# Optimization experiments

Hardware: AMD Instinct MI355X
Metric: run time of the kernel (lower is better)

The kernel has to match this reference:

```python
import jax, jax.numpy as jnp
import numpy as np
from jax import lax

ENC_DIM, DEC_DIM, ATT_DIM, CONV_CH, KSIZE, ATT_ODIM = 1024, 1024, 512, 32, 50, 1024
SCALING = 2.0


def setup_inputs() -> dict:
    key = jax.random.key(0)
    ks = jax.random.split(key, 12)
    B, T = 32, 2000
    enc_pad = jax.random.normal(ks[0], (B, T, ENC_DIM), dtype=jnp.float32)
    enc_len = jax.random.randint(ks[1], (B,), 1000, T + 1, dtype=jnp.int32)
    dec_h = jax.random.normal(ks[2], (B, 1, DEC_DIM), dtype=jnp.float32)
    att_prev = jax.random.uniform(ks[3], (B, T), dtype=jnp.float32)
    s = 0.02
    W_enc = jax.random.normal(ks[4], (ENC_DIM, ATT_DIM), dtype=jnp.float32) * s
    b_enc = jnp.zeros((ATT_DIM,), jnp.float32)
    W_dec = jax.random.normal(ks[5], (DEC_DIM, ATT_DIM), dtype=jnp.float32) * s
    b_dec = jnp.zeros((ATT_DIM,), jnp.float32)
    W_att = jax.random.normal(ks[6], (CONV_CH, ATT_DIM), dtype=jnp.float32) * s
    b_att = jnp.zeros((ATT_DIM,), jnp.float32)
    # Conv2d(1, C, kernel=(1, 2K+1)) acting on (B,1,1,T) == 1D conv kernel (C,1,2K+1)
    conv_w = jax.random.normal(ks[7], (CONV_CH, 1, 2 * KSIZE + 1), dtype=jnp.float32) * s
    gvec = jax.random.normal(ks[8], (ATT_DIM, 1), dtype=jnp.float32) * s
    W_o = jax.random.normal(ks[9], (ENC_DIM, ATT_ODIM), dtype=jnp.float32) * s
    b_o = jnp.zeros((ATT_ODIM,), jnp.float32)
    return {"enc_pad": enc_pad, "enc_len": enc_len, "dec_h": dec_h, "att_prev": att_prev,
            "W_enc": W_enc, "b_enc": b_enc, "W_dec": W_dec, "b_dec": b_dec,
            "W_att": W_att, "b_att": b_att, "conv_w": conv_w, "gvec": gvec,
            "W_o": W_o, "b_o": b_o}


def reference(enc_pad, enc_len, dec_h, att_prev, W_enc, b_enc, W_dec, b_dec,
              W_att, b_att, conv_w, gvec, W_o, b_o):
    B, T, _ = enc_pad.shape
    enc_h = enc_pad @ W_enc + b_enc                           # [B,T,A]
    # location conv: (B,1,T) * (C,1,K) -> (B,C,T), SAME padding
    att_conv = lax.conv_general_dilated(
        att_prev[:, None, :], conv_w, window_strides=(1,),
        padding=[(KSIZE, KSIZE)], dimension_numbers=("NCH", "OIH", "NCH"))
    att_conv = jnp.transpose(att_conv, (0, 2, 1)) @ W_att + b_att  # [B,T,A]
    dec_term = (dec_h.reshape(B, DEC_DIM) @ W_dec + b_dec)[:, None, :]  # [B,1,A]
    att_state = jnp.tanh(enc_h + dec_term + att_conv)         # [B,T,A]
    e = (att_state @ gvec)[:, :, 0]                           # [B,T]
    mask = jnp.arange(T)[None, :] >= enc_len[:, None]         # True = padded
    e = jnp.where(mask, jnp.float32(-1e15), e)
    attn = jax.nn.softmax(SCALING * e, axis=1)                # [B,T]
    c = jnp.einsum("bt,btd->bd", attn, enc_pad)               # [B,enc_dim]
    c = c @ W_o + b_o                                         # [B,att_odim]
    return c, attn
```

## Files before the change

### kernel.cpp

```cpp
#include <hip/hip_runtime.h>
#include <stdint.h>
#include <stddef.h>

#define T_LEN   2000
#define BATCH   32
#define ROWS    64000
#define KDIM    1024
#define ADIM    512
#define CCH     32
#define KW      101

typedef _Float16 half8_t  __attribute__((ext_vector_type(8)));
typedef _Float16 half4_t  __attribute__((ext_vector_type(4)));
typedef float    float4_t __attribute__((ext_vector_type(4)));

__device__ __forceinline__ half8_t pack8(float4_t a, float4_t b) {
    half8_t r;
    r[0] = (_Float16)a.x; r[1] = (_Float16)a.y;
    r[2] = (_Float16)a.z; r[3] = (_Float16)a.w;
    r[4] = (_Float16)b.x; r[5] = (_Float16)b.y;
    r[6] = (_Float16)b.z; r[7] = (_Float16)b.w;
    return r;
}

__device__ __forceinline__ float tanh_fast(float x) {
    float ax = __builtin_fabsf(x);
    ax = fminf(ax, 15.f);
    float e = __expf(2.f * ax);
    float t = 1.f - 2.f * __builtin_amdgcn_rcpf(e + 1.f);
    return (x < 0.f) ? -t : t;
}

__device__ __forceinline__ void glds16(const void* g, void* l) {
    __builtin_amdgcn_global_load_lds((const __attribute__((address_space(1))) uint32_t*)g,
                                     (__attribute__((address_space(3))) uint32_t*)l,
                                     16, 0, 0);
}

#define OFF_WENCT 0
#define OFF_WATTT 1048576
#define OFF_CONV  1081344
#define M_DTERM   5177344
#define M_EPART   5242880
#define M_CPART   6266880
#define M_ENCH    8364032
#define F_DTERM   9273344
#define F_EPART   9338880
#define F_CPART   10362880

__global__ __launch_bounds__(256) void k_prep(const float* __restrict__ We,
                                              const float* __restrict__ Wa,
                                              const float* __restrict__ dec_h,
                                              const float* __restrict__ W_dec,
                                              const float* __restrict__ be,
                                              const float* __restrict__ bd,
                                              const float* __restrict__ ba,
                                              const float* __restrict__ att_prev,
                                              const float* __restrict__ conv_w,
                                              const float* __restrict__ enc,
                                              _Float16* __restrict__ Wet,
                                              _Float16* __restrict__ Wat,
                                              float* __restrict__ dterm,
                                              void* __restrict__ convO,
                                              _Float16* __restrict__ encH,
                                              int f16mode) {
    __shared__ float smem[3460];
    const int blk = blockIdx.x, tid = threadIdx.x;

    if (blk >= 1153) {
        const size_t idx = (size_t)(blk - 1153) * 2048 + tid * 8;
        const float4_t* s = (const float4_t*)(enc + idx);
        float4_t v0 = s[0], v1 = s[1];
        *(half8_t*)(encH + idx) = pack8(v0, v1);
        return;
    }
    if (blk < 512) {
        float (*tile)[33] = (float(*)[33])smem;
        const int k0 = (blk >> 4) * 32, n0 = (blk & 15) * 32;
        const int tx = tid & 31, ty = tid >> 5;
#pragma unroll
        for (int i = 0; i < 4; ++i)
            tile[ty + i * 8][tx] = We[(size_t)(k0 + ty + i * 8) * ADIM + n0 + tx];
        __syncthreads();
#pragma unroll
        for (int i = 0; i < 4; ++i)
            Wet[(size_t)(n0 + ty + i * 8) * KDIM + k0 + tx] = (_Float16)tile[tx][ty + i * 8];
    } else if (blk < 640) {
        float* dh = smem;
        float* part = smem + 1024;
        const int idx = blk - 512, b = idx >> 2, a0 = (idx & 3) * 128;
#pragma unroll
        for (int i = 0; i < 4; ++i) dh[tid + i * 256] = dec_h[b * KDIM + tid + i * 256];
        __syncthreads();
        const int a = a0 + (tid & 127), kh = (tid >> 7) * 512;
        float s = 0.f;
#pragma unroll 8
        for (int k = 0; k < 512; ++k) s += dh[kh + k] * W_dec[(size_t)(kh + k) * ADIM + a];
        part[tid] = s;
        __syncthreads();
        if (tid < 128) {
            const int aa = a0 + tid;
            dterm[b * ADIM + aa] = part[tid] + part[tid + 128] + be[aa] + bd[aa] + ba[aa];
        }
    } else if (blk < 1152) {
        float* ap = smem;
        float* w  = smem + 228;
        const int idx = blk - 640, b = idx >> 4, tt = idx & 15;
        const int t0 = tt * 128;
        for (int i = tid; i < 228; i += 256) {
            int t = t0 - 50 + i;
            ap[i] = (t >= 0 && t < T_LEN) ? att_prev[b * T_LEN + t] : 0.f;
        }
        for (int i = tid; i < CCH * KW; i += 256) w[i] = conv_w[i];
        __syncthreads();
        for (int idx2 = tid; idx2 < 128 * CCH; idx2 += 256) {
            int tl = idx2 >> 5, c = idx2 & 31;
            int t = t0 + tl;
            if (t < T_LEN) {
                float s = 0.f;
#pragma unroll
                for (int j = 0; j < KW; ++j) s += ap[tl + j] * w[c * KW + j];
                const size_t o = (size_t)(b * T_LEN + t) * CCH + c;
                if (f16mode) ((_Float16*)convO)[o] = (_Float16)s;
                else         ((float*)convO)[o] = s;
            }
        }
    } else {
#pragma unroll
        for (int rr = 0; rr < 2; ++rr) {
            const int n = tid * 2 + rr;
#pragma unroll
            for (int c = 0; c < CCH; ++c)
                Wat[n * CCH + c] = (_Float16)Wa[c * ADIM + n];
        }
    }
}

template<bool F16A>
__global__ __launch_bounds__(256, F16A ? 4 : 3)
void k_gemm_e(const void* __restrict__ encv,
              const _Float16* __restrict__ Wet,
              const void* __restrict__ convv,
              const _Float16* __restrict__ Wat,
              const float* __restrict__ dterm,
              const float* __restrict__ gvec,
              float* __restrict__ epart) {
    constexpr int ABYTES = F16A ? 8192 : 16384;
    __shared__ __attribute__((aligned(16))) char     Ab[2][ABYTES];
    __shared__ __attribute__((aligned(16))) _Float16 Bh[2][128 * 32];

    const int tid  = threadIdx.x;
    const int blk  = blockIdx.x;
    int nc, mt;
    if (blk < 1984) { nc = (blk >> 3) & 3; mt = (blk >> 5) * 8 + (blk & 7); }
    else            { int r = blk - 1984; nc = r >> 2; mt = 496 + (r & 3); }
    const int m0 = mt * 128, n0 = nc * 128;

    const int wave = tid >> 6, lane = tid & 63;
    const int quad = lane >> 4, c16 = lane & 15;
    const int wm = (wave >> 1) * 64, wn = (wave & 1) * 64;

    const int rlB = lane & 15, sgB = lane >> 4;
    const int rlA = F16A ? (lane & 15) : (lane & 7);
    const int sgA = F16A ? (lane >> 4) : (lane >> 3);
    constexpr int AISS = F16A ? 2 : 4;
    constexpr int ARPC = F16A ? 16 : 8;
    constexpr int AEPS = F16A ? 8 : 4;

    const _Float16* encH = (const _Float16*)encv;
    const float*    encF = (const float*)encv;
    const _Float16* cvH  = (const _Float16*)convv;
    const float*    cvF  = (const float*)convv;

    const size_t aRow = (size_t)(m0 + wave * 32 + rlA);
    const size_t bRow = (size_t)(n0 + wave * 32 + rlB);

    float g[4], dt0[4], dt1[4];
    const int b0 = m0 / T_LEN, b1 = (m0 + 127) / T_LEN;
    const int lim = (b0 + 1) * T_LEN;
#pragma unroll
    for (int j = 0; j < 4; ++j) {
        const int col = n0 + wn + j * 16 + c16;
        g[j]   = gvec[col];
        dt0[j] = dterm[b0 * ADIM + col];
        dt1[j] = dterm[b1 * ADIM + col];
    }

    float4_t acc[4][4];
#pragma unroll
    for (int i = 0; i < 4; ++i)
#pragma unroll
        for (int j = 0; j < 4; ++j) acc[i][j] = (float4_t){0.f, 0.f, 0.f, 0.f};

#define STAGE_A(buf, base, stride, k0)                                              \
    _Pragma("unroll")                                                               \
    for (int i = 0; i < AISS; ++i)                                                  \
        glds16((base) + ((aRow + i * ARPC) * (stride)) + (k0) + sgA * AEPS,         \
               &Ab[buf][(wave * AISS + i) * 1024]);
#define STAGE_B(buf, base, stride, k0)                                              \
    _Pragma("unroll")                                                               \
    for (int i = 0; i < 2; ++i)                                                     \
        glds16((base) + ((bRow + i * 16) * (stride)) + (k0) + sgB * 8,              \
               (char*)&Bh[buf][0] + (wave * 2 + i) * 1024);

    if (F16A) { STAGE_A(0, encH, KDIM, 0) } else { STAGE_A(0, encF, KDIM, 0) }
    STAGE_B(0, Wet, KDIM, 0)
    __syncthreads();

    for (int kk = 0; kk < 33; ++kk) {
        const int cur = kk & 1, nxt = cur ^ 1;
        if (kk < 31) {
            const int kn = (kk + 1) * 32;
            if (F16A) { STAGE_A(nxt, encH, KDIM, kn) } else { STAGE_A(nxt, encF, KDIM, kn) }
            STAGE_B(nxt, Wet, KDIM, kn)
        } else if (kk == 31) {
            if (F16A) { STAGE_A(nxt, cvH, CCH, 0) } else { STAGE_A(nxt, cvF, CCH, 0) }
            STAGE_B(nxt, Wat, CCH, 0)
        }
        half8_t af[4], bf[4];
        if (F16A) {
            const _Float16* Ah = (const _Float16*)Ab[cur];
#pragma unroll
            for (int i = 0; i < 4; ++i) {
                const int row = wm + i * 16 + c16;
                af[i] = *(const half8_t*)(Ah + (row >> 4) * 512 + (quad * 16 + c16) * 8);
            }
        } else {
            const float* Afp = (const float*)Ab[cur];
#pragma unroll
            for (int i = 0; i < 4; ++i) {
                const int row = wm + i * 16 + c16;
                const float* cb = Afp + (row >> 3) * 256 + (row & 7) * 4;
                float4_t u0 = *(const float4_t*)(cb + (2 * quad) * 32);
                float4_t u1 = *(const float4_t*)(cb + (2 * quad + 1) * 32);
                af[i] = pack8(u0, u1);
            }
        }
#pragma unroll
        for (int j = 0; j < 4; ++j) {
            const int row = wn + j * 16 + c16;
            bf[j] = *(const half8_t*)(&Bh[cur][0] + (row >> 4) * 512 + (quad * 16 + c16) * 8);
        }
#pragma unroll
        for (int i = 0; i < 4; ++i)
#pragma unroll
            for (int j = 0; j < 4; ++j)
                acc[i][j] = __builtin_amdgcn_mfma_f32_16x16x32_f16(af[i], bf[j], acc[i][j], 0, 0, 0);
        __syncthreads();
    }

    float* e_lds = (float*)&Bh[0][0];
#pragma unroll
    for (int i = 0; i < 4; ++i) {
#pragma unroll
        for (int r = 0; r < 4; ++r) {
            const int rloc = wm + i * 16 + quad * 4 + r;
            const bool hi = (m0 + rloc) >= lim;
            float s = 0.f;
#pragma unroll
            for (int j = 0; j < 4; ++j)
                s += tanh_fast(acc[i][j][r] + (hi ? dt1[j] : dt0[j])) * g[j];
#pragma unroll
            for (int off = 1; off < 16; off <<= 1) s += __shfl_xor(s, off);
            if (c16 == 0) e_lds[rloc * 2 + (wave & 1)] = s;
        }
    }
    __syncthreads();
    if (tid < 128) {
        const float2 q = ((const float2*)e_lds)[tid];
        epart[nc * ROWS + m0 + tid] = q.x + q.y;
    }
#undef STAGE_A
#undef STAGE_B
}

__global__ __launch_bounds__(512) void k_softmax(const float* __restrict__ epart,
                                                 const int* __restrict__ enc_len,
                                                 float* __restrict__ attn) {
    __shared__ float ex[T_LEN];
    __shared__ float red[8];
    const int b = blockIdx.x, tid = threadIdx.x;
    const int len = enc_len[b];
    float lmax = -3.4e38f;
    for (int t = tid; t < T_LEN; t += 512) {
        float e = epart[b * T_LEN + t] + epart[ROWS + b * T_LEN + t]
                + epart[2 * ROWS + b * T_LEN + t] + epart[3 * ROWS + b * T_LEN + t];
        float lg = (t < len) ? 2.f * e : -2e15f;
        ex[t] = lg;
        lmax = fmaxf(lmax, lg);
    }
    for (int off = 1; off < 64; off <<= 1) lmax = fmaxf(lmax, __shfl_xor(lmax, off));
    if ((tid & 63) == 0) red[tid >> 6] = lmax;
    __syncthreads();
    const float m = fmaxf(fmaxf(fmaxf(red[0], red[1]), fmaxf(red[2], red[3])),
                          fmaxf(fmaxf(red[4], red[5]), fmaxf(red[6], red[7])));
    float lsum = 0.f;
    for (int t = tid; t < T_LEN; t += 512) {
        float p = __expf(ex[t] - m);
        ex[t] = p;
        lsum += p;
    }
    for (int off = 1; off < 64; off <<= 1) lsum += __shfl_xor(lsum, off);
    __syncthreads();
    if ((tid & 63) == 0) red[tid >> 6] = lsum;
    __syncthreads();
    const float inv = 1.f / (red[0] + red[1] + red[2] + red[3] + red[4] + red[5] + red[6] + red[7]);
    for (int t = tid; t < T_LEN; t += 512) attn[b * T_LEN + t] = ex[t] * inv;
}

__global__ __launch_bounds__(256) void k_cpart_h(const float* __restrict__ attn,
                                                 const _Float16* __restrict__ encH,
                                                 float* __restrict__ cpart) {
    const int b = blockIdx.y, tc = blockIdx.x, tid = threadIdx.x;
    const int t0 = tc * 125;
    float4_t s = (float4_t){0.f, 0.f, 0.f, 0.f};
    const half4_t* ep = (const half4_t*)(encH + (size_t)b * T_LEN * KDIM) + tid;
    const float* ap = attn + b * T_LEN + t0;
#pragma unroll 5
    for (int tt = 0; tt < 125; ++tt) {
        const float w = ap[tt];
        half4_t v = ep[(size_t)(t0 + tt) * 256];
        s.x += w * (float)v[0]; s.y += w * (float)v[1];
        s.z += w * (float)v[2]; s.w += w * (float)v[3];
    }
    *(float4_t*)&cpart[(size_t)(tc * BATCH + b) * KDIM + tid * 4] = s;
}

__global__ __launch_bounds__(256) void k_cpart_f(const float* __restrict__ attn,
                                                 const float* __restrict__ enc,
                                                 float* __restrict__ cpart) {
    const int b = blockIdx.y, tc = blockIdx.x, tid = threadIdx.x;
    const int t0 = tc * 125;
    float4_t s = (float4_t){0.f, 0.f, 0.f, 0.f};
    const float4_t* ep = (const float4_t*)(enc + (size_t)b * T_LEN * KDIM) + tid;
    const float* ap = attn + b * T_LEN + t0;
#pragma unroll 5
    for (int tt = 0; tt < 125; ++tt) {
        const float w = ap[tt];
        float4_t v = ep[(size_t)(t0 + tt) * 256];
        s += v * w;
    }
    *(float4_t*)&cpart[(size_t)(tc * BATCH + b) * KDIM + tid * 4] = s;
}

__global__ __launch_bounds__(256) void k_out(const float* __restrict__ cpart,
                                             const float* __restrict__ W_o,
                                             const float* __restrict__ b_o,
                                             float* __restrict__ out_c) {
    __shared__ float cm[KDIM];
    const int b = blockIdx.x, tid = threadIdx.x;
    for (int d = tid; d < KDIM; d += 256) {
        float s = 0.f;
#pragma unroll
        for (int p = 0; p < 16; ++p) s += cpart[(size_t)(p * BATCH + b) * KDIM + d];
        cm[d] = s;
    }
    __syncthreads();
    const int o = blockIdx.y * 256 + tid;
    float s = b_o[o];
#pragma unroll 8
    for (int d = 0; d < KDIM; ++d) s += cm[d] * W_o[(size_t)d * KDIM + o];
    out_c[b * KDIM + o] = s;
}

extern "C" void kernel_launch(void* const* d_in, const int* in_sizes, int n_in,
                              void* d_out, int out_size, void* d_ws, size_t ws_size,
                              hipStream_t stream) {
    const float* enc      = (const float*)d_in[0];
    const int*   enc_len  = (const int*)d_in[1];
    const float* dec_h    = (const float*)d_in[2];
    const float* att_prev = (const float*)d_in[3];
    const float* W_enc    = (const float*)d_in[4];
    const float* b_enc    = (const float*)d_in[5];
    const float* W_dec    = (const float*)d_in[6];
    const float* b_dec    = (const float*)d_in[7];
    const float* W_att    = (const float*)d_in[8];
    const float* b_att    = (const float*)d_in[9];
    const float* conv_w   = (const float*)d_in[10];
    const float* gvec     = (const float*)d_in[11];
    const float* W_o      = (const float*)d_in[12];
    const float* b_o      = (const float*)d_in[13];

    float* out_c    = (float*)d_out;
    float* out_attn = out_c + BATCH * KDIM;

    char* ws = (char*)d_ws;
    _Float16* Wet = (_Float16*)(ws + OFF_WENCT);
    _Float16* Wat = (_Float16*)(ws + OFF_WATTT);

    const size_t needMain = (size_t)M_ENCH + (size_t)ROWS * KDIM * 2;
    const bool f16p = ws_size >= needMain;

    if (f16p) {
        _Float16* convH = (_Float16*)(ws + OFF_CONV);
        float*    dterm = (float*)(ws + M_DTERM);
        float*    epart = (float*)(ws + M_EPART);
        float*    cpart = (float*)(ws + M_CPART);
        _Float16* encH  = (_Float16*)(ws + M_ENCH);

        k_prep<<<1153 + 32000, 256, 0, stream>>>(W_enc, W_att, dec_h, W_dec, b_enc, b_dec,
                                                 b_att, att_prev, conv_w, enc,
                                                 Wet, Wat, dterm, convH, encH, 1);
        k_gemm_e<true><<<2000, 256, 0, stream>>>(encH, Wet, convH, Wat, dterm, gvec, epart);
        k_softmax<<<BATCH, 512, 0, stream>>>(epart, enc_len, out_attn);
        k_cpart_h<<<dim3(16, BATCH), 256, 0, stream>>>(out_attn, encH, cpart);
        k_out<<<dim3(BATCH, 4), 256, 0, stream>>>(cpart, W_o, b_o, out_c);
    } else {
        float* convF = (float*)(ws + OFF_CONV);
        float* dterm = (float*)(ws + F_DTERM);
        float* epart = (float*)(ws + F_EPART);
        float* cpart = (float*)(ws + F_CPART);

        k_prep<<<1153, 256, 0, stream>>>(W_enc, W_att, dec_h, W_dec, b_enc, b_dec,
                                         b_att, att_prev, conv_w, enc,
                                         Wet, Wat, dterm, convF, (_Float16*)nullptr, 0);
        k_gemm_e<false><<<2000, 256, 0, stream>>>(enc, Wet, convF, Wat, dterm, gvec, epart);
        k_softmax<<<BATCH, 512, 0, stream>>>(epart, enc_len, out_attn);
        k_cpart_f<<<dim3(16, BATCH), 256, 0, stream>>>(out_attn, enc, cpart);
        k_out<<<dim3(BATCH, 4), 256, 0, stream>>>(cpart, W_o, b_o, out_c);
    }
}
```

Measured before the change: 611.9 us.

## Triple-buffer fp16 GEMM pipeline with vmcnt waits and coarsen fp16 conversion blocks

The fp16 GEMM path becomes a dedicated kernel with three LDS stages, two stages prefetched ahead. It waits with explicit s_waitcnt vmcnt plus a raw barrier instead of a full __syncthreads per K step, so global loads overlap more MFMA work. The fp32 fallback is split into its own kernel. The enc fp32-to-fp16 conversion blocks each handle four chunks, cutting that launch from 32000 to 8000 blocks. The larger LDS footprint (48KB) may lower occupancy, and the hand-placed vmcnt counts must match the number of glds16 issues per stage.

```diff
diff --git a/kernel.cpp b/kernel.cpp
--- a/kernel.cpp
+++ b/kernel.cpp
@@ -68,10 +68,13 @@
     const int blk = blockIdx.x, tid = threadIdx.x;
 
     if (blk >= 1153) {
-        const size_t idx = (size_t)(blk - 1153) * 2048 + tid * 8;
-        const float4_t* s = (const float4_t*)(enc + idx);
-        float4_t v0 = s[0], v1 = s[1];
-        *(half8_t*)(encH + idx) = pack8(v0, v1);
+        const size_t base = (size_t)(blk - 1153) * 8192 + (size_t)tid * 8;
+#pragma unroll
+        for (int i = 0; i < 4; ++i) {
+            const size_t idx = base + (size_t)i * 2048;
+            const float4_t* s = (const float4_t*)(enc + idx);
+            *(half8_t*)(encH + idx) = pack8(s[0], s[1]);
+        }
         return;
     }
     if (blk < 512) {
@@ -136,18 +139,16 @@
     }
 }
 
-template<bool F16A>
-__global__ __launch_bounds__(256, F16A ? 4 : 3)
-void k_gemm_e(const void* __restrict__ encv,
-              const _Float16* __restrict__ Wet,
-              const void* __restrict__ convv,
-              const _Float16* __restrict__ Wat,
-              const float* __restrict__ dterm,
-              const float* __restrict__ gvec,
-              float* __restrict__ epart) {
-    constexpr int ABYTES = F16A ? 8192 : 16384;
-    __shared__ __attribute__((aligned(16))) char     Ab[2][ABYTES];
-    __shared__ __attribute__((aligned(16))) _Float16 Bh[2][128 * 32];
+__global__ __launch_bounds__(256, 3)
+void k_gemm3(const _Float16* __restrict__ encH,
+             const _Float16* __restrict__ Wet,
+             const _Float16* __restrict__ cvH,
+             const _Float16* __restrict__ Wat,
+             const float* __restrict__ dterm,
+             const float* __restrict__ gvec,
+             float* __restrict__ epart) {
+    __shared__ __attribute__((aligned(16))) char     Ab[3][8192];
+    __shared__ __attribute__((aligned(16))) _Float16 Bh[3][4096];
 
     const int tid  = threadIdx.x;
     const int blk  = blockIdx.x;
@@ -159,21 +160,10 @@
     const int wave = tid >> 6, lane = tid & 63;
     const int quad = lane >> 4, c16 = lane & 15;
     const int wm = (wave >> 1) * 64, wn = (wave & 1) * 64;
-
-    const int rlB = lane & 15, sgB = lane >> 4;
-    const int rlA = F16A ? (lane & 15) : (lane & 7);
-    const int sgA = F16A ? (lane >> 4) : (lane >> 3);
-    constexpr int AISS = F16A ? 2 : 4;
-    constexpr int ARPC = F16A ? 16 : 8;
-    constexpr int AEPS = F16A ? 8 : 4;
-
-    const _Float16* encH = (const _Float16*)encv;
-    const float*    encF = (const float*)encv;
-    const _Float16* cvH  = (const _Float16*)convv;
-    const float*    cvF  = (const float*)convv;
-
-    const size_t aRow = (size_t)(m0 + wave * 32 + rlA);
-    const size_t bRow = (size_t)(n0 + wave * 32 + rlB);
+    const int rl = lane & 15, sg = lane >> 4;
+
+    const size_t aRow = (size_t)(m0 + wave * 32 + rl);
+    const size_t bRow = (size_t)(n0 + wave * 32 + rl);
 
     float g[4], dt0[4], dt1[4];
     const int b0 = m0 / T_LEN, b1 = (m0 + 127) / T_LEN;
@@ -192,18 +182,141 @@
 #pragma unroll
         for (int j = 0; j < 4; ++j) acc[i][j] = (float4_t){0.f, 0.f, 0.f, 0.f};
 
+#define STG(bf, s)                                                                  \
+    {                                                                               \
+        if ((s) < 32) {                                                             \
+            const int kn = (s) * 32;                                                \
+            _Pragma("unroll")                                                       \
+            for (int i = 0; i < 2; ++i)                                             \
+                glds16(encH + (aRow + (size_t)(i * 16)) * KDIM + kn + sg * 8,       \
+                       &Ab[bf][(wave * 2 + i) * 1024]);                             \
+            _Pragma("unroll")                                                       \
+            for (int i = 0; i < 2; ++i)                                             \
+                glds16(Wet + (bRow + (size_t)(i * 16)) * KDIM + kn + sg * 8,        \
+                       (char*)&Bh[bf][0] + (wave * 2 + i) * 1024);                  \
+        } else {                                                                    \
+            _Pragma("unroll")                                                       \
+            for (int i = 0; i < 2; ++i)                                             \
+                glds16(cvH + (aRow + (size_t)(i * 16)) * CCH + sg * 8,              \
+                       &Ab[bf][(wave * 2 + i) * 1024]);                             \
+            _Pragma("unroll")                                                       \
+            for (int i = 0; i < 2; ++i)                                             \
+                glds16(Wat + (bRow + (size_t)(i * 16)) * CCH + sg * 8,              \
+                       (char*)&Bh[bf][0] + (wave * 2 + i) * 1024);                  \
+        }                                                                           \
+    }
+
+    STG(0, 0)
+    STG(1, 1)
+
+    for (int kk = 0; kk < 33; ++kk) {
+        if (kk < 32) asm volatile("s_waitcnt vmcnt(4)" ::: "memory");
+        else         asm volatile("s_waitcnt vmcnt(0)" ::: "memory");
+        __builtin_amdgcn_s_barrier();
+        __builtin_amdgcn_sched_barrier(0);
+
+        const int s = kk + 2;
+        if (s <= 32) { const int bf = s - (s / 3) * 3; STG(bf, s) }
+
+        const int cur = kk - (kk / 3) * 3;
+        const _Float16* Ah = (const _Float16*)Ab[cur];
+        const _Float16* Bp = &Bh[cur][0];
+        half8_t af[4], bf4[4];
+#pragma unroll
+        for (int i = 0; i < 4; ++i)
+            af[i] = *(const half8_t*)(Ah + ((wm + i * 16) >> 4) * 512 + lane * 8);
+#pragma unroll
+        for (int j = 0; j < 4; ++j)
+            bf4[j] = *(const half8_t*)(Bp + ((wn + j * 16) >> 4) * 512 + lane * 8);
+#pragma unroll
+        for (int i = 0; i < 4; ++i)
+#pragma unroll
+            for (int j = 0; j < 4; ++j)
+                acc[i][j] = __builtin_amdgcn_mfma_f32_16x16x32_f16(af[i], bf4[j], acc[i][j], 0, 0, 0);
+    }
+#undef STG
+    __syncthreads();
+
+    float* e_lds = (float*)&Bh[0][0];
+#pragma unroll
+    for (int i = 0; i < 4; ++i) {
+#pragma unroll
+        for (int r = 0; r < 4; ++r) {
+            const int rloc = wm + i * 16 + quad * 4 + r;
+            const bool hi = (m0 + rloc) >= lim;
+            float s = 0.f;
+#pragma unroll
+            for (int j = 0; j < 4; ++j)
+                s += tanh_fast(acc[i][j][r] + (hi ? dt1[j] : dt0[j])) * g[j];
+#pragma unroll
+            for (int off = 1; off < 16; off <<= 1) s += __shfl_xor(s, off);
+            if (c16 == 0) e_lds[rloc * 2 + (wave & 1)] = s;
+        }
+    }
+    __syncthreads();
+    if (tid < 128) {
+        const float2 q = ((const float2*)e_lds)[tid];
+        epart[nc * ROWS + m0 + tid] = q.x + q.y;
+    }
+}
+
+__global__ __launch_bounds__(256, 3)
+void k_gemm_f(const float* __restrict__ encF,
+              const _Float16* __restrict__ Wet,
+              const float* __restrict__ cvF,
+              const _Float16* __restrict__ Wat,
+              const float* __restrict__ dterm,
+              const float* __restrict__ gvec,
+              float* __restrict__ epart) {
+    __shared__ __attribute__((aligned(16))) char     Ab[2][16384];
+    __shared__ __attribute__((aligned(16))) _Float16 Bh[2][128 * 32];
+
+    const int tid  = threadIdx.x;
+    const int blk  = blockIdx.x;
+    int nc, mt;
+    if (blk < 1984) { nc = (blk >> 3) & 3; mt = (blk >> 5) * 8 + (blk & 7); }
+    else            { int r = blk - 1984; nc = r >> 2; mt = 496 + (r & 3); }
+    const int m0 = mt * 128, n0 = nc * 128;
+
+    const int wave = tid >> 6, lane = tid & 63;
+    const int quad = lane >> 4, c16 = lane & 15;
+    const int wm = (wave >> 1) * 64, wn = (wave & 1) * 64;
+
+    const int rlB = lane & 15, sgB = lane >> 4;
+    const int rlA = lane & 7,  sgA = lane >> 3;
+
+    const size_t aRow = (size_t)(m0 + wave * 32 + rlA);
+    const size_t bRow = (size_t)(n0 + wave * 32 + rlB);
+
+    float g[4], dt0[4], dt1[4];
+    const int b0 = m0 / T_LEN, b1 = (m0 + 127) / T_LEN;
+    const int lim = (b0 + 1) * T_LEN;
+#pragma unroll
+    for (int j = 0; j < 4; ++j) {
+        const int col = n0 + wn + j * 16 + c16;
+        g[j]   = gvec[col];
+        dt0[j] = dterm[b0 * ADIM + col];
+        dt1[j] = dterm[b1 * ADIM + col];
+    }
+
+    float4_t acc[4][4];
+#pragma unroll
+    for (int i = 0; i < 4; ++i)
+#pragma unroll
+        for (int j = 0; j < 4; ++j) acc[i][j] = (float4_t){0.f, 0.f, 0.f, 0.f};
+
 #define STAGE_A(buf, base, stride, k0)                                              \
     _Pragma("unroll")                                                               \
-    for (int i = 0; i < AISS; ++i)                                                  \
-        glds16((base) + ((aRow + i * ARPC) * (stride)) + (k0) + sgA * AEPS,         \
-               &Ab[buf][(wave * AISS + i) * 1024]);
+    for (int i = 0; i < 4; ++i)                                                     \
+        glds16((base) + ((aRow + i * 8) * (stride)) + (k0) + sgA * 4,               \
+               &Ab[buf][(wave * 4 + i) * 1024]);
 #define STAGE_B(buf, base, stride, k0)                                              \
     _Pragma("unroll")                                                               \
     for (int i = 0; i < 2; ++i)                                                     \
         glds16((base) + ((bRow + i * 16) * (stride)) + (k0) + sgB * 8,              \
                (char*)&Bh[buf][0] + (wave * 2 + i) * 1024);
 
-    if (F16A) { STAGE_A(0, encH, KDIM, 0) } else { STAGE_A(0, encF, KDIM, 0) }
+    STAGE_A(0, encF, KDIM, 0)
     STAGE_B(0, Wet, KDIM, 0)
     __syncthreads();
 
@@ -211,30 +324,21 @@
         const int cur = kk & 1, nxt = cur ^ 1;
         if (kk < 31) {
             const int kn = (kk + 1) * 32;
-            if (F16A) { STAGE_A(nxt, encH, KDIM, kn) } else { STAGE_A(nxt, encF, KDIM, kn) }
+            STAGE_A(nxt, encF, KDIM, kn)
             STAGE_B(nxt, Wet, KDIM, kn)
         } else if (kk == 31) {
-            if (F16A) { STAGE_A(nxt, cvH, CCH, 0) } else { STAGE_A(nxt, cvF, CCH, 0) }
+            STAGE_A(nxt, cvF, CCH, 0)
             STAGE_B(nxt, Wat, CCH, 0)
         }
         half8_t af[4], bf[4];
-        if (F16A) {
-            const _Float16* Ah = (const _Float16*)Ab[cur];
-#pragma unroll
-            for (int i = 0; i < 4; ++i) {
-                const int row = wm + i * 16 + c16;
-                af[i] = *(const half8_t*)(Ah + (row >> 4) * 512 + (quad * 16 + c16) * 8);
-            }
-        } else {
-            const float* Afp = (const float*)Ab[cur];
-#pragma unroll
-            for (int i = 0; i < 4; ++i) {
-                const int row = wm + i * 16 + c16;
-                const float* cb = Afp + (row >> 3) * 256 + (row & 7) * 4;
-                float4_t u0 = *(const float4_t*)(cb + (2 * quad) * 32);
-                float4_t u1 = *(const float4_t*)(cb + (2 * quad + 1) * 32);
-                af[i] = pack8(u0, u1);
-            }
+        const float* Afp = (const float*)Ab[cur];
+#pragma unroll
+        for (int i = 0; i < 4; ++i) {
+            const int row = wm + i * 16 + c16;
+            const float* cb = Afp + (row >> 3) * 256 + (row & 7) * 4;
+            float4_t u0 = *(const float4_t*)(cb + (2 * quad) * 32);
+            float4_t u1 = *(const float4_t*)(cb + (2 * quad + 1) * 32);
+            af[i] = pack8(u0, u1);
         }
 #pragma unroll
         for (int j = 0; j < 4; ++j) {
@@ -248,6 +352,8 @@
                 acc[i][j] = __builtin_amdgcn_mfma_f32_16x16x32_f16(af[i], bf[j], acc[i][j], 0, 0, 0);
         __syncthreads();
     }
+#undef STAGE_A
+#undef STAGE_B
 
     float* e_lds = (float*)&Bh[0][0];
 #pragma unroll
@@ -270,8 +376,6 @@
         const float2 q = ((const float2*)e_lds)[tid];
         epart[nc * ROWS + m0 + tid] = q.x + q.y;
     }
-#undef STAGE_A
-#undef STAGE_B
 }
 
 __global__ __launch_bounds__(512) void k_softmax(const float* __restrict__ epart,
@@ -398,10 +502,10 @@
         float*    cpart = (float*)(ws + M_CPART);
         _Float16* encH  = (_Float16*)(ws + M_ENCH);
 
-        k_prep<<<1153 + 32000, 256, 0, stream>>>(W_enc, W_att, dec_h, W_dec, b_enc, b_dec,
-                                                 b_att, att_prev, conv_w, enc,
-                                                 Wet, Wat, dterm, convH, encH, 1);
-        k_gemm_e<true><<<2000, 256, 0, stream>>>(encH, Wet, convH, Wat, dterm, gvec, epart);
+        k_prep<<<1153 + 8000, 256, 0, stream>>>(W_enc, W_att, dec_h, W_dec, b_enc, b_dec,
+                                                b_att, att_prev, conv_w, enc,
+                                                Wet, Wat, dterm, convH, encH, 1);
+        k_gemm3<<<2000, 256, 0, stream>>>(encH, Wet, convH, Wat, dterm, gvec, epart);
         k_softmax<<<BATCH, 512, 0, stream>>>(epart, enc_len, out_attn);
         k_cpart_h<<<dim3(16, BATCH), 256, 0, stream>>>(out_attn, encH, cpart);
         k_out<<<dim3(BATCH, 4), 256, 0, stream>>>(cpart, W_o, b_o, out_c);
@@ -414,7 +518,7 @@
         k_prep<<<1153, 256, 0, stream>>>(W_enc, W_att, dec_h, W_dec, b_enc, b_dec,
                                          b_att, att_prev, conv_w, enc,
                                          Wet, Wat, dterm, convF, (_Float16*)nullptr, 0);
-        k_gemm_e<false><<<2000, 256, 0, stream>>>(enc, Wet, convF, Wat, dterm, gvec, epart);
+        k_gemm_f<<<2000, 256, 0, stream>>>(enc, Wet, convF, Wat, dterm, gvec, epart);
         k_softmax<<<BATCH, 512, 0, stream>>>(epart, enc_len, out_attn);
         k_cpart_f<<<dim3(16, BATCH), 256, 0, stream>>>(out_attn, enc, cpart);
         k_out<<<dim3(BATCH, 4), 256, 0, stream>>>(cpart, W_o, b_o, out_c);
```

Measured after the change: 637.0 us. +4.1%, slower.

## Add triple-buffered direct-to-LDS fp16 GEMM kernel for attention energies

Applied to the files above, without the earlier changes.

Replaces the fp16 energy GEMM with a new kernel that stages A tiles into a three-slot LDS ring and B tiles into a double buffer, using direct global-to-LDS loads. Only one barrier is taken per k-step, and the conv/W_att contribution is folded in as a 33rd k-step. The aim is deeper prefetch, so that global latency is hidden behind the MFMA work. The extra LDS buffer raises shared memory use per block, and the vmcnt accounting must stay correct for the pipeline to remain valid.

```diff
diff --git a/kernel.cpp b/kernel.cpp
--- a/kernel.cpp
+++ b/kernel.cpp
@@ -136,6 +136,135 @@
     }
 }
 
+__global__ __launch_bounds__(256, 4)
+void k_gemm_p(const _Float16* __restrict__ encH,
+              const _Float16* __restrict__ Wet,
+              const _Float16* __restrict__ cvH,
+              const _Float16* __restrict__ Wat,
+              const float* __restrict__ dterm,
+              const float* __restrict__ gvec,
+              float* __restrict__ epart) {
+    __shared__ __attribute__((aligned(16))) char Ab[3][8192];
+    __shared__ __attribute__((aligned(16))) char Bh[2][8192];
+
+    const int tid  = threadIdx.x;
+    const int blk  = blockIdx.x;
+    int nc, mt;
+    if (blk < 1984) { nc = (blk >> 3) & 3; mt = (blk >> 5) * 8 + (blk & 7); }
+    else            { int r = blk - 1984; nc = r >> 2; mt = 496 + (r & 3); }
+    const int m0 = mt * 128, n0 = nc * 128;
+
+    const int wave = tid >> 6, lane = tid & 63;
+    const int quad = lane >> 4, c16 = lane & 15;
+    const int wm = (wave >> 1) * 64, wn = (wave & 1) * 64;
+    const int rl = lane & 15, sg = lane >> 4;
+
+    const size_t aRow = (size_t)(m0 + wave * 32 + rl);
+    const size_t bRow = (size_t)(n0 + wave * 32 + rl);
+
+    float g[4], dt0[4], dt1[4];
+    const int b0 = m0 / T_LEN, b1 = (m0 + 127) / T_LEN;
+    const int lim = (b0 + 1) * T_LEN;
+#pragma unroll
+    for (int j = 0; j < 4; ++j) {
+        const int col = n0 + wn + j * 16 + c16;
+        g[j]   = gvec[col];
+        dt0[j] = dterm[b0 * ADIM + col];
+        dt1[j] = dterm[b1 * ADIM + col];
+    }
+
+    float4_t acc[4][4];
+#pragma unroll
+    for (int i = 0; i < 4; ++i)
+#pragma unroll
+        for (int j = 0; j < 4; ++j) acc[i][j] = (float4_t){0.f, 0.f, 0.f, 0.f};
+
+#define STG_A(s)                                                                     \
+    {                                                                                \
+        const int bf = (s) - ((s) / 3) * 3;                                          \
+        if ((s) < 32) {                                                              \
+            const int kn = (s) * 32;                                                 \
+            glds16(encH + (aRow +  0) * KDIM + kn + sg * 8, &Ab[bf][(wave*2+0)*1024]); \
+            glds16(encH + (aRow + 16) * KDIM + kn + sg * 8, &Ab[bf][(wave*2+1)*1024]); \
+        } else {                                                                     \
+            glds16(cvH + (aRow +  0) * CCH + sg * 8, &Ab[bf][(wave*2+0)*1024]);      \
+            glds16(cvH + (aRow + 16) * CCH + sg * 8, &Ab[bf][(wave*2+1)*1024]);      \
+        }                                                                            \
+    }
+#define STG_B(s)                                                                     \
+    {                                                                                \
+        const int bf = (s) & 1;                                                      \
+        if ((s) < 32) {                                                              \
+            const int kn = (s) * 32;                                                 \
+            glds16(Wet + (bRow +  0) * KDIM + kn + sg * 8, &Bh[bf][(wave*2+0)*1024]); \
+            glds16(Wet + (bRow + 16) * KDIM + kn + sg * 8, &Bh[bf][(wave*2+1)*1024]); \
+        } else {                                                                     \
+            glds16(Wat + (bRow +  0) * CCH + sg * 8, &Bh[bf][(wave*2+0)*1024]);      \
+            glds16(Wat + (bRow + 16) * CCH + sg * 8, &Bh[bf][(wave*2+1)*1024]);      \
+        }                                                                            \
+    }
+
+    STG_B(0)
+    STG_A(0)
+    STG_A(1)
+
+    for (int kk = 0; kk < 33; ++kk) {
+        if (kk < 32) asm volatile("s_waitcnt vmcnt(2)" ::: "memory");
+        else         asm volatile("s_waitcnt vmcnt(0)" ::: "memory");
+        __builtin_amdgcn_s_barrier();
+        __builtin_amdgcn_sched_barrier(0);
+
+        if (kk + 1 <= 32) STG_B(kk + 1)
+        if (kk + 2 <= 32) STG_A(kk + 2)
+
+        const int cur3 = kk - (kk / 3) * 3;
+        const int cur2 = kk & 1;
+        const _Float16* Ah = (const _Float16*)Ab[cur3];
+        const _Float16* Bp = (const _Float16*)Bh[cur2];
+        half8_t af[4], bf4[4];
+#pragma unroll
+        for (int i = 0; i < 4; ++i) {
+            const int row = wm + i * 16 + c16;
+            af[i] = *(const half8_t*)(Ah + (row >> 4) * 512 + (quad * 16 + c16) * 8);
+        }
+#pragma unroll
+        for (int j = 0; j < 4; ++j) {
+            const int row = wn + j * 16 + c16;
+            bf4[j] = *(const half8_t*)(Bp + (row >> 4) * 512 + (quad * 16 + c16) * 8);
+        }
+#pragma unroll
+        for (int i = 0; i < 4; ++i)
+#pragma unroll
+            for (int j = 0; j < 4; ++j)
+                acc[i][j] = __builtin_amdgcn_mfma_f32_16x16x32_f16(af[i], bf4[j], acc[i][j], 0, 0, 0);
+    }
+#undef STG_A
+#undef STG_B
+    __syncthreads();
+
+    float* e_lds = (float*)&Bh[0][0];
+#pragma unroll
+    for (int i = 0; i < 4; ++i) {
+#pragma unroll
+        for (int r = 0; r < 4; ++r) {
+            const int rloc = wm + i * 16 + quad * 4 + r;
+            const bool hi = (m0 + rloc) >= lim;
+            float s = 0.f;
+#pragma unroll
+            for (int j = 0; j < 4; ++j)
+                s += tanh_fast(acc[i][j][r] + (hi ? dt1[j] : dt0[j])) * g[j];
+#pragma unroll
+            for (int off = 1; off < 16; off <<= 1) s += __shfl_xor(s, off);
+            if (c16 == 0) e_lds[rloc * 2 + (wave & 1)] = s;
+        }
+    }
+    __syncthreads();
+    if (tid < 128) {
+        const float2 q = ((const float2*)e_lds)[tid];
+        epart[nc * ROWS + m0 + tid] = q.x + q.y;
+    }
+}
+
 template<bool F16A>
 __global__ __launch_bounds__(256, F16A ? 4 : 3)
 void k_gemm_e(const void* __restrict__ encv,
@@ -401,7 +530,7 @@
         k_prep<<<1153 + 32000, 256, 0, stream>>>(W_enc, W_att, dec_h, W_dec, b_enc, b_dec,
                                                  b_att, att_prev, conv_w, enc,
                                                  Wet, Wat, dterm, convH, encH, 1);
-        k_gemm_e<true><<<2000, 256, 0, stream>>>(encH, Wet, convH, Wat, dterm, gvec, epart);
+        k_gemm_p<<<2000, 256, 0, stream>>>(encH, Wet, convH, Wat, dterm, gvec, epart);
         k_softmax<<<BATCH, 512, 0, stream>>>(epart, enc_len, out_attn);
         k_cpart_h<<<dim3(16, BATCH), 256, 0, stream>>>(out_attn, encH, cpart);
         k_out<<<dim3(BATCH, 4), 256, 0, stream>>>(cpart, W_o, b_o, out_c);
```

Measured after the change: 607.5 us. About the same (-0.7%).
